# Optimization experiments

Hardware: AMD Instinct MI355X
Metric: run time of the kernel (lower is better)

Reference implementation:

```python
import jax, jax.numpy as jnp
import numpy as np

JOINT = 512
VID_DIM = 1024
K_SIZE = 4
STRIDE = 2
LAYERS = 6
START_LAYER = 1
MARGIN = 0.2
NMS_K = 5          # greedy NMS picks per (query, video) row
NMS_THRESH = 0.7   # IoU suppression threshold
NEG = -1e9


def l2norm(x, axis=-1, eps=1e-8):
    return x / (jnp.linalg.norm(x, axis=axis, keepdims=True) + eps)


def conv1d(x, w, stride):
    # x: [B, C, T], w: [O, I, K] -> [B, O, T']
    return jax.lax.conv_general_dilated(
        x, w, (stride,), 'VALID', dimension_numbers=('NCH', 'OIH', 'NCH'))


def setup_inputs() -> dict:
    key = jax.random.key(0)
    ks = jax.random.split(key, 12)
    B, T, L = 32, 256, 20
    # proposal count P from the valid-conv pyramid
    t, P = T, 0
    for i in range(LAYERS):
        t = (t - K_SIZE) // STRIDE + 1
        if i >= START_LAYER - 1:
            P += t
    video = jax.random.normal(ks[0], (B, T, VID_DIM), jnp.float32)
    words = jax.random.normal(ks[1], (B, L, JOINT), jnp.float32)
    w_masks = jnp.ones((B, L), jnp.bool_)
    lam = jax.random.uniform(ks[2], (1,), jnp.float32)
    iou = jax.random.uniform(ks[3], (P, P), jnp.float32)
    iou_map = 0.5 * (iou + iou.T)  # symmetric pairwise IoU
    scale = 0.02
    fc_w = scale * jax.random.normal(ks[4], (JOINT, VID_DIM), jnp.float32)
    fc_b = jnp.zeros((JOINT,), jnp.float32)
    conv_w = scale * jax.random.normal(ks[5], (LAYERS, JOINT, JOINT, K_SIZE), jnp.float32)
    conv_b = jnp.zeros((LAYERS, JOINT), jnp.float32)
    pw = scale * jax.random.normal(ks[6], (JOINT, JOINT, 1), jnp.float32)
    pb = jnp.zeros((JOINT,), jnp.float32)
    return {'video': video, 'words': words, 'w_masks': w_masks, 'lam': lam,
            'iou_map': iou_map, 'fc_w': fc_w, 'fc_b': fc_b,
            'conv_w': conv_w, 'conv_b': conv_b, 'pw': pw, 'pb': pb}


def diag_loss(scores, margin):
    b = scores.shape[0]
    d = jnp.diag(scores)[:, None]
    cost_s = jnp.clip(margin + scores - d, 0.0)
    cost_im = jnp.clip(margin + scores - d.T, 0.0)
    eye = jnp.eye(b, dtype=bool)
    cost_s = jnp.where(eye, 0.0, cost_s)
    cost_im = jnp.where(eye, 0.0, cost_im)
    return cost_s.sum() / b + cost_im.sum() / b


def _forward(video, words, w_masks, lam, iou_map, fc_w, fc_b, conv_w, conv_b, pw, pb):
    v = jnp.einsum('btv,jv->btj', video, fc_w) + fc_b      # fc: [B,T,J]
    v = jnp.transpose(v, (0, 2, 1))                         # [B,J,T]
    sims = []
    for li in range(LAYERS):
        v = jax.nn.relu(conv1d(v, conv_w[li], STRIDE) + conv_b[li][None, :, None])
        if li >= START_LAYER - 1:
            f = conv1d(v, pw, 1) + pb[None, :, None]        # conv_1d projection
            f = jnp.transpose(f, (0, 2, 1))                 # [B,Tl,J]
            # frame_by_word: frames attend to each query's words (all pairs at once)
            att = jnp.einsum('btd,qld->qbtl', f, words)     # [Q,B,Tl,L]
            att = jnp.where(w_masks[:, None, None, :], att, NEG)
            att = jax.nn.softmax(att, axis=-1)
            v_s = jnp.einsum('qbtl,qld->qbtd', att, words)  # [Q,B,Tl,J]
            sim = jnp.sum(l2norm(f)[None] * l2norm(v_s), axis=-1)  # cosine, [Q,B,Tl]
            sims.append(sim)
    score = jnp.concatenate(sims, axis=-1)                  # [Q,B,P]
    B = score.shape[0]
    positive_map = score[jnp.arange(B), jnp.arange(B)]      # [B,P]
    lam0 = lam[0]

    def nms_row(row):  # greedy temporal NMS scoring over P proposals
        def step(s, k):
            idx = jnp.argmax(s)
            val = jnp.max(s)
            w = lam0 ** k.astype(jnp.float32)
            s = jnp.where(iou_map[idx] > NMS_THRESH, NEG, s)
            s = s.at[idx].set(NEG)
            return s, val * w
        _, vals = jax.lax.scan(step, row, jnp.arange(NMS_K))
        return jnp.sum(vals) / NMS_K

    scores_mat = jax.vmap(jax.vmap(nms_row))(score)         # [Q,B]
    loss = diag_loss(scores_mat, MARGIN)
    return loss, positive_map


def reference(video, words, w_masks, lam, iou_map, fc_w, fc_b, conv_w, conv_b, pw, pb):
    return _forward(video, words, w_masks, lam, iou_map, fc_w, fc_b, conv_w, conv_b, pw, pb)
```

## Files before the change

kernel.cpp:

```cpp
#include <hip/hip_runtime.h>
#include <math.h>

#define B_   32
#define T0_  256
#define J_   512
#define V_   1024
#define Q_   32
#define L_   20
#define P_   241
#define NEG_ (-1e9f)

typedef __attribute__((ext_vector_type(8))) _Float16 half8;
typedef __attribute__((ext_vector_type(4))) _Float16 half4v;
typedef __attribute__((ext_vector_type(4))) float f32x4;

template<int BM, int EPI>
__global__ __launch_bounds__(256) void g1p(
    const _Float16* __restrict__ AH, const _Float16* __restrict__ BH,
    const float* __restrict__ bias,
    _Float16* __restrict__ outH, float* __restrict__ outF,
    int MROWS, int TDIV, int SB, int S0, int TMUL, int BSTR,
    int KLEN, int MP, int OSB, int OS0, int NS) {
  constexpr int FM = BM / 32;
  constexpr int APT = BM / 32;
  constexpr int TPRA = 256 / BM;
  __shared__ _Float16 aS[BM * 72], bS[64 * 72];

  const int tid = threadIdx.x;
  const int m0 = blockIdx.x * BM, n0 = blockIdx.y * 64;
  const int k00 = blockIdx.z * KLEN;
  const int wave = tid >> 6, lane = tid & 63;
  const int wm = (wave >> 1) * (BM / 2), wn = (wave & 1) * 32;
  const int fr = lane & 15, fq = lane >> 4;

  const int arow = tid / TPRA;
  const int acol = (tid % TPRA) * (APT * 8);
  const int brow = tid >> 2, bcol = (tid & 3) * 16;

  const int gm = m0 + arow;
  const bool mval = gm < MROWS;
  const int b2g = gm / TDIV, t2g = gm - b2g * TDIV;
  const size_t aoff = (size_t)(b2g * SB + S0 + t2g * TMUL) * 512;
  const size_t boff = (size_t)(n0 + brow) * (size_t)BSTR;

  f32x4 acc[FM][2];
  #pragma unroll
  for (int i = 0; i < FM; ++i) {
    acc[i][0] = (f32x4)0.f;
    acc[i][1] = (f32x4)0.f;
  }

  half8 z;
  #pragma unroll
  for (int j = 0; j < 8; ++j) z[j] = (_Float16)0.f;

  half8 rA[APT], rB[2];
  auto load = [&](int it) {
    const int k = k00 + it * 64;
    if (mval) {
      #pragma unroll
      for (int i = 0; i < APT; ++i)
        rA[i] = *reinterpret_cast<const half8*>(&AH[aoff + k + acol + i * 8]);
    } else {
      #pragma unroll
      for (int i = 0; i < APT; ++i) rA[i] = z;
    }
    rB[0] = *reinterpret_cast<const half8*>(&BH[boff + k + bcol]);
    rB[1] = *reinterpret_cast<const half8*>(&BH[boff + k + bcol + 8]);
  };

  load(0);
  const int NI = KLEN >> 6;

  for (int it = 0; it < NI; ++it) {
    __syncthreads();
    #pragma unroll
    for (int i = 0; i < APT; ++i)
      *reinterpret_cast<half8*>(&aS[arow * 72 + acol + i * 8]) = rA[i];
    *reinterpret_cast<half8*>(&bS[brow * 72 + bcol]) = rB[0];
    *reinterpret_cast<half8*>(&bS[brow * 72 + bcol + 8]) = rB[1];
    __syncthreads();
    if (it + 1 < NI) load(it + 1);

    #pragma unroll
    for (int ks = 0; ks < 2; ++ks) {
      const int ko = ks * 32 + fq * 8;
      half8 a[FM], b[2];
      #pragma unroll
      for (int mt = 0; mt < FM; ++mt)
        a[mt] = *reinterpret_cast<const half8*>(&aS[(wm + mt * 16 + fr) * 72 + ko]);
      b[0] = *reinterpret_cast<const half8*>(&bS[(wn + fr) * 72 + ko]);
      b[1] = *reinterpret_cast<const half8*>(&bS[(wn + 16 + fr) * 72 + ko]);
      #pragma unroll
      for (int mt = 0; mt < FM; ++mt) {
        acc[mt][0] = __builtin_amdgcn_mfma_f32_16x16x32_f16(a[mt], b[0], acc[mt][0], 0, 0, 0);
        acc[mt][1] = __builtin_amdgcn_mfma_f32_16x16x32_f16(a[mt], b[1], acc[mt][1], 0, 0, 0);
      }
    }
  }

  #pragma unroll
  for (int mt = 0; mt < FM; ++mt) {
    const int mB2 = m0 + wm + mt * 16 + fq * 4;
    #pragma unroll
    for (int nt = 0; nt < 2; ++nt) {
      const int n = n0 + wn + nt * 16 + fr;
      f32x4 c = acc[mt][nt];
      #pragma unroll
      for (int r = 0; r < 4; ++r) {
        const int m = mB2 + r;
        if (m < MROWS) {
          if (EPI == 3) {
            outF[((size_t)blockIdx.z * MP + m) * 512 + n] = c[r];
          } else if (EPI == 2) {
            outF[(size_t)m * NS + n] = c[r];
          } else {
            float x = c[r] + bias[n];
            if (EPI == 1) x = fmaxf(x, 0.f);
            const int bb2 = m / TDIV, tt2 = m - bb2 * TDIV;
            const int orow = bb2 * OSB + OS0 + tt2;
            outH[(size_t)orow * 512 + n] = (_Float16)x;
          }
        }
      }
    }
  }
}

__global__ __launch_bounds__(256) void fc1p(
    const float* __restrict__ A, const _Float16* __restrict__ BH,
    const float* __restrict__ bias, _Float16* __restrict__ outH) {
  __shared__ _Float16 aS[128 * 72], bS[64 * 72];
  const int tid = threadIdx.x;
  const int m0 = blockIdx.x * 128, n0 = blockIdx.y * 64;
  const int wave = tid >> 6, lane = tid & 63;
  const int wm = (wave >> 1) * 64, wn = (wave & 1) * 32;
  const int fr = lane & 15, fq = lane >> 4;
  const int arow = tid >> 1, acol = (tid & 1) * 32;
  const int brow = tid >> 2, bcol = (tid & 3) * 16;
  const size_t aoff = (size_t)(m0 + arow) * 1024;
  const size_t boff = (size_t)(n0 + brow) * 1024;

  f32x4 acc[4][2];
  #pragma unroll
  for (int i = 0; i < 4; ++i) { acc[i][0] = (f32x4)0.f; acc[i][1] = (f32x4)0.f; }

  float4 rAf[8];
  half8 rB[2];
  auto load = [&](int it) {
    const int k = it * 64;
    const float* pa = &A[aoff + k + acol];
    #pragma unroll
    for (int i = 0; i < 8; ++i) rAf[i] = *reinterpret_cast<const float4*>(pa + i * 4);
    rB[0] = *reinterpret_cast<const half8*>(&BH[boff + k + bcol]);
    rB[1] = *reinterpret_cast<const half8*>(&BH[boff + k + bcol + 8]);
  };

  load(0);
  for (int it = 0; it < 16; ++it) {
    __syncthreads();
    #pragma unroll
    for (int g = 0; g < 4; ++g) {
      float tf[8];
      *reinterpret_cast<float4*>(tf) = rAf[2 * g];
      *reinterpret_cast<float4*>(tf + 4) = rAf[2 * g + 1];
      half8 h8;
      #pragma unroll
      for (int j = 0; j < 8; ++j) h8[j] = (_Float16)tf[j];
      *reinterpret_cast<half8*>(&aS[arow * 72 + acol + g * 8]) = h8;
    }
    *reinterpret_cast<half8*>(&bS[brow * 72 + bcol]) = rB[0];
    *reinterpret_cast<half8*>(&bS[brow * 72 + bcol + 8]) = rB[1];
    __syncthreads();
    if (it + 1 < 16) load(it + 1);

    #pragma unroll
    for (int ks = 0; ks < 2; ++ks) {
      const int ko = ks * 32 + fq * 8;
      half8 a[4], b[2];
      #pragma unroll
      for (int mt = 0; mt < 4; ++mt)
        a[mt] = *reinterpret_cast<const half8*>(&aS[(wm + mt * 16 + fr) * 72 + ko]);
      b[0] = *reinterpret_cast<const half8*>(&bS[(wn + fr) * 72 + ko]);
      b[1] = *reinterpret_cast<const half8*>(&bS[(wn + 16 + fr) * 72 + ko]);
      #pragma unroll
      for (int mt = 0; mt < 4; ++mt) {
        acc[mt][0] = __builtin_amdgcn_mfma_f32_16x16x32_f16(a[mt], b[0], acc[mt][0], 0, 0, 0);
        acc[mt][1] = __builtin_amdgcn_mfma_f32_16x16x32_f16(a[mt], b[1], acc[mt][1], 0, 0, 0);
      }
    }
  }

  #pragma unroll
  for (int mt = 0; mt < 4; ++mt) {
    const int mB2 = m0 + wm + mt * 16 + fq * 4;
    #pragma unroll
    for (int nt = 0; nt < 2; ++nt) {
      const int n = n0 + wn + nt * 16 + fr;
      f32x4 c = acc[mt][nt];
      #pragma unroll
      for (int r = 0; r < 4; ++r) {
        const int m = mB2 + r;
        outH[(size_t)m * 512 + n] = (_Float16)(c[r] + bias[n]);
      }
    }
  }
}

__global__ __launch_bounds__(256) void reduce_kernel(
    const float* __restrict__ part, const float* __restrict__ bias,
    _Float16* __restrict__ outH,
    int kS, int MROWS, int MP, int Tl, int Poff) {
  int idx = blockIdx.x * 256 + threadIdx.x;
  if (idx >= MROWS * 512) return;
  int m = idx >> 9, n = idx & 511;
  float s = 0.f;
  for (int ks = 0; ks < kS; ++ks) s += part[((size_t)ks * MP + m) * 512 + n];
  float x = fmaxf(s + bias[n], 0.f);
  int b2 = m / Tl, t2 = m - b2 * Tl;
  int orow = b2 * P_ + Poff + t2;
  outH[(size_t)orow * 512 + n] = (_Float16)x;
}

__global__ __launch_bounds__(256) void split_h(
    const float* __restrict__ a, const float* __restrict__ b,
    const float* __restrict__ c,
    _Float16* __restrict__ oa, _Float16* __restrict__ ob,
    _Float16* __restrict__ oc) {
  int i = blockIdx.x * 256 + threadIdx.x;
  const float* src; _Float16* dst; int off;
  if (i < 131072)      { src = a; dst = oa; off = i; }
  else if (i < 196608) { src = b; dst = ob; off = i - 131072; }
  else if (i < 278528) { src = c; dst = oc; off = i - 196608; }
  else return;
  float4 v = *reinterpret_cast<const float4*>(&src[(size_t)off * 4]);
  half4v h;
  h[0] = (_Float16)v.x; h[1] = (_Float16)v.y;
  h[2] = (_Float16)v.z; h[3] = (_Float16)v.w;
  *reinterpret_cast<half4v*>(&dst[(size_t)off * 4]) = h;
}

__global__ __launch_bounds__(256) void repack_h(
    const float* __restrict__ w, _Float16* __restrict__ oh) {
  int e = blockIdx.x * 256 + threadIdx.x;
  if (e >= 6 * 512 * 512) return;
  float4 v = *reinterpret_cast<const float4*>(&w[(size_t)e * 4]);
  int li = e >> 18, rem = e & 262143, o = rem >> 9, i = rem & 511;
  size_t rb = ((size_t)(li * 512 + o)) * 2048 + i;
  oh[rb]        = (_Float16)v.x;
  oh[rb + 512]  = (_Float16)v.y;
  oh[rb + 1024] = (_Float16)v.z;
  oh[rb + 1536] = (_Float16)v.w;
}

__global__ __launch_bounds__(256) void fnorm_kernel(
    const _Float16* __restrict__ fH, float* __restrict__ fn) {
  int gw = (blockIdx.x * 256 + threadIdx.x) >> 6;
  int lane = threadIdx.x & 63;
  if (gw >= B_ * P_) return;
  half8 h = *reinterpret_cast<const half8*>(&fH[(size_t)gw * 512 + lane * 8]);
  float s = 0.f;
  #pragma unroll
  for (int j = 0; j < 8; ++j) {
    float x = (float)h[j];
    s += x * x;
  }
  #pragma unroll
  for (int off = 32; off; off >>= 1) s += __shfl_xor(s, off);
  if (lane == 0) fn[gw] = sqrtf(s);
}

__global__ __launch_bounds__(256) void gram_kernel(
    const float* __restrict__ words, float* __restrict__ gram) {
  __shared__ float wsh[L_][513];
  int q = blockIdx.x, tid = threadIdx.x;
  for (int idx = tid; idx < L_ * 512; idx += 256)
    wsh[idx >> 9][idx & 511] = words[(size_t)q * L_ * J_ + idx];
  __syncthreads();
  for (int pr = tid; pr < L_ * L_; pr += 256) {
    int l = pr / L_, l2 = pr % L_;
    float sum = 0.f;
    for (int d = 0; d < J_; ++d) sum += wsh[l][d] * wsh[l2][d];
    gram[q * L_ * L_ + pr] = sum;
  }
}

__global__ __launch_bounds__(256) void sim_kernel(
    const float* __restrict__ logits, const float* __restrict__ gram,
    const float* __restrict__ fnorm, float* __restrict__ score) {
  int idx = blockIdx.x * 256 + threadIdx.x;
  if (idx >= Q_ * B_ * P_) return;
  int q = idx / (B_ * P_);
  int r = idx - q * (B_ * P_);
  const float* lg = &logits[(size_t)r * (Q_ * L_) + q * L_];
  float raw[L_], e[L_];
  float m = -1e30f;
  #pragma unroll
  for (int l = 0; l < L_; ++l) { raw[l] = lg[l]; m = fmaxf(m, raw[l]); }
  float s = 0.f;
  #pragma unroll
  for (int l = 0; l < L_; ++l) { e[l] = __expf(raw[l] - m); s += e[l]; }
  float inv = 1.f / s;
  float fvs = 0.f;
  #pragma unroll
  for (int l = 0; l < L_; ++l) fvs += e[l] * raw[l];
  fvs *= inv;
  const float* G = &gram[q * L_ * L_];
  float vn2 = 0.f;
  for (int l = 0; l < L_; ++l) {
    float acc = 0.f;
    #pragma unroll
    for (int l2 = 0; l2 < L_; ++l2) acc += e[l2] * G[l * L_ + l2];
    vn2 += e[l] * acc;
  }
  vn2 *= inv * inv;
  float fn = fnorm[r] + 1e-8f;
  float vn = sqrtf(fmaxf(vn2, 0.f)) + 1e-8f;
  score[idx] = fvs / (fn * vn);
}

__global__ __launch_bounds__(256) void nms_kernel(
    const float* __restrict__ score, const float* __restrict__ iou,
    const float* __restrict__ lam, float* __restrict__ smat) {
  int wid = (blockIdx.x * 256 + threadIdx.x) >> 6;
  int lane = threadIdx.x & 63;
  if (wid >= Q_ * B_) return;
  const float* srow = &score[(size_t)wid * P_];
  float s[4];
  #pragma unroll
  for (int i = 0; i < 4; ++i) {
    int p = lane + 64 * i;
    s[i] = (p < P_) ? srow[p] : NEG_;
  }
  float lamv = lam[0];
  float acc = 0.f, wgt = 1.f;
  for (int k = 0; k < 5; ++k) {
    float bv = NEG_ * 2.f; int bi = 1 << 30;
    #pragma unroll
    for (int i = 0; i < 4; ++i) {
      int p = lane + 64 * i;
      if (s[i] > bv) { bv = s[i]; bi = p; }
    }
    for (int off = 32; off; off >>= 1) {
      float ov = __shfl_xor(bv, off);
      int oi = __shfl_xor(bi, off);
      if (ov > bv || (ov == bv && oi < bi)) { bv = ov; bi = oi; }
    }
    acc += bv * wgt;
    wgt *= lamv;
    const float* irow = &iou[(size_t)bi * P_];
    #pragma unroll
    for (int i = 0; i < 4; ++i) {
      int p = lane + 64 * i;
      if (p < P_ && irow[p] > 0.7f) s[i] = NEG_;
      if (p == bi) s[i] = NEG_;
    }
  }
  if (lane == 0) smat[wid] = acc * 0.2f;
}

__global__ __launch_bounds__(256) void posmap_kernel(
    const float* __restrict__ score, float* __restrict__ out) {
  int idx = blockIdx.x * 256 + threadIdx.x;
  if (idx >= B_ * P_) return;
  int b = idx / P_, p = idx - b * P_;
  out[1 + idx] = score[((size_t)(b * B_ + b)) * P_ + p];
}

__global__ __launch_bounds__(1024) void loss_kernel(
    const float* __restrict__ smat, float* __restrict__ out) {
  __shared__ float sm[B_][B_ + 1];
  __shared__ float red[16];
  int tid = threadIdx.x;
  sm[tid >> 5][tid & 31] = smat[tid];
  __syncthreads();
  int i = tid >> 5, j = tid & 31;
  float val = 0.f;
  if (i != j) {
    float sij = sm[i][j];
    val = fmaxf(0.f, 0.2f + sij - sm[i][i]) + fmaxf(0.f, 0.2f + sij - sm[j][j]);
  }
  #pragma unroll
  for (int off = 32; off; off >>= 1) val += __shfl_xor(val, off);
  if ((tid & 63) == 0) red[tid >> 6] = val;
  __syncthreads();
  if (tid == 0) {
    float t = 0.f;
    #pragma unroll
    for (int w = 0; w < 16; ++w) t += red[w];
    out[0] = t / 32.f;
  }
}

extern "C" void kernel_launch(void* const* d_in, const int* in_sizes, int n_in,
                              void* d_out, int out_size, void* d_ws, size_t ws_size,
                              hipStream_t stream) {
  const float* video  = (const float*)d_in[0];
  const float* words  = (const float*)d_in[1];
  const float* lam    = (const float*)d_in[3];
  const float* iou    = (const float*)d_in[4];
  const float* fc_w   = (const float*)d_in[5];
  const float* fc_b   = (const float*)d_in[6];
  const float* conv_w = (const float*)d_in[7];
  const float* conv_b = (const float*)d_in[8];
  const float* pw     = (const float*)d_in[9];
  const float* pb     = (const float*)d_in[10];
  float* out = (float*)d_out;

  char* base = (char*)d_ws;
  _Float16* fcoH  = (_Float16*)(base + 0);
  _Float16* pyrH  = (_Float16*)(base + 8388608);
  _Float16* fallH = (_Float16*)(base + 16285696);
  _Float16* cwH   = (_Float16*)(base + 24182784);
  _Float16* fcwH  = (_Float16*)(base + 36765696);
  _Float16* pwH   = (_Float16*)(base + 37814272);
  _Float16* wordsH= (_Float16*)(base + 38338560);
  float*    logits= (float*)(base + 38993920);
  float*    part  = (float*)(base + 38993920);
  float*    score = (float*)(base + 58736640);
  float*    fnorm = (float*)(base + 59723776);
  float*    gram  = (float*)(base + 59755520);
  float*    smat  = (float*)(base + 59806720);

  const int Tl[6]   = {127, 62, 30, 14, 6, 2};
  const int Poff[6] = {0, 127, 189, 219, 233, 239};

  split_h<<<1088, 256, 0, stream>>>(fc_w, pw, words, fcwH, pwH, wordsH);
  repack_h<<<6144, 256, 0, stream>>>(conv_w, cwH);

  fc1p<<<dim3(64, 8), 256, 0, stream>>>(video, fcwH, fc_b, fcoH);

  g1p<64, 1><<<dim3(64, 8, 1), 256, 0, stream>>>(
      fcoH, cwH, conv_b, pyrH, nullptr,
      4064, 127, 256, 0, 2, 2048, 2048, 0, P_, 0, 512);

  const int Ms[5]    = {1984, 960, 448, 192, 64};
  const int mbs[5]   = {31, 15, 7, 3, 1};
  const int kSs[5]   = {2, 4, 4, 8, 8};
  const int KLENs[5] = {1024, 512, 512, 256, 256};
  for (int i = 0; i < 5; ++i) {
    int li = i + 1;
    g1p<64, 3><<<dim3(mbs[i], 8, kSs[i]), 256, 0, stream>>>(
        pyrH, cwH + (size_t)li * 512 * 2048, nullptr, nullptr, part,
        Ms[i], Tl[li], P_, Poff[li - 1], 2, 2048, KLENs[i], Ms[i], 0, 0, 512);
    reduce_kernel<<<Ms[i] * 2, 256, 0, stream>>>(
        part, conv_b + li * 512, pyrH, kSs[i], Ms[i], Ms[i], Tl[li], Poff[li]);
  }

  g1p<128, 0><<<dim3(61, 8, 1), 256, 0, stream>>>(
      pyrH, pwH, pb, fallH, nullptr,
      B_ * P_, B_ * P_, 0, 0, 1, 512, 512, 0, 0, 0, 512);

  fnorm_kernel<<<1928, 256, 0, stream>>>(fallH, fnorm);
  gram_kernel<<<Q_, 256, 0, stream>>>(words, gram);
  g1p<128, 2><<<dim3(61, 10, 1), 256, 0, stream>>>(
      fallH, wordsH, nullptr, nullptr, logits,
      B_ * P_, B_ * P_, 0, 0, 1, 512, 512, 0, 0, 0, 640);

  sim_kernel<<<964, 256, 0, stream>>>(logits, gram, fnorm, score);

  nms_kernel<<<256, 256, 0, stream>>>(score, iou, lam, smat);
  posmap_kernel<<<31, 256, 0, stream>>>(score, out);
  loss_kernel<<<1, 1024, 0, stream>>>(smat, out);
}
```

Before: 213.8 us.

## Generalize GEMM K-chunk to 128, replace fused-convert FC GEMM with pre-conversion

The GEMM kernel gains a K-chunk template parameter and an explicit A row stride. All GEMMs now use 128-wide K chunks, which halves the number of barrier/load iterations. The special FC kernel that converted fp32 video on the fly is removed. Instead a separate pass converts video to fp16, and the generic GEMM then runs with BM=64 over a larger grid. The projection and logits GEMMs also switch from BM=128 to BM=64, giving twice as many blocks. In exchange there is an extra 32MB read plus 16MB write for the conversion, and shared memory use per block doubles.

```diff
diff --git a/kernel.cpp b/kernel.cpp
--- a/kernel.cpp
+++ b/kernel.cpp
@@ -14,17 +14,21 @@
 typedef __attribute__((ext_vector_type(4))) _Float16 half4v;
 typedef __attribute__((ext_vector_type(4))) float f32x4;
 
-template<int BM, int EPI>
+template<int BM, int KCH, int EPI>
 __global__ __launch_bounds__(256) void g1p(
     const _Float16* __restrict__ AH, const _Float16* __restrict__ BH,
     const float* __restrict__ bias,
     _Float16* __restrict__ outH, float* __restrict__ outF,
-    int MROWS, int TDIV, int SB, int S0, int TMUL, int BSTR,
+    int MROWS, int TDIV, int SB, int S0, int TMUL, int ASTR, int BSTR,
     int KLEN, int MP, int OSB, int OS0, int NS) {
   constexpr int FM = BM / 32;
-  constexpr int APT = BM / 32;
+  constexpr int LSTR = KCH + 8;
   constexpr int TPRA = 256 / BM;
-  __shared__ _Float16 aS[BM * 72], bS[64 * 72];
+  constexpr int AW = KCH / TPRA;
+  constexpr int AU = AW / 8;
+  constexpr int BW = KCH / 4;
+  constexpr int BU = BW / 8;
+  __shared__ _Float16 aS[BM * LSTR], bS[64 * LSTR];
 
   const int tid = threadIdx.x;
   const int m0 = blockIdx.x * BM, n0 = blockIdx.y * 64;
@@ -34,63 +38,62 @@
   const int fr = lane & 15, fq = lane >> 4;
 
   const int arow = tid / TPRA;
-  const int acol = (tid % TPRA) * (APT * 8);
-  const int brow = tid >> 2, bcol = (tid & 3) * 16;
+  const int acol = (tid % TPRA) * AW;
+  const int brow = tid >> 2, bcol = (tid & 3) * BW;
 
   const int gm = m0 + arow;
   const bool mval = gm < MROWS;
   const int b2g = gm / TDIV, t2g = gm - b2g * TDIV;
-  const size_t aoff = (size_t)(b2g * SB + S0 + t2g * TMUL) * 512;
+  const size_t aoff = (size_t)(b2g * SB + S0 + t2g * TMUL) * (size_t)ASTR;
   const size_t boff = (size_t)(n0 + brow) * (size_t)BSTR;
 
   f32x4 acc[FM][2];
   #pragma unroll
-  for (int i = 0; i < FM; ++i) {
-    acc[i][0] = (f32x4)0.f;
-    acc[i][1] = (f32x4)0.f;
-  }
+  for (int i = 0; i < FM; ++i) { acc[i][0] = (f32x4)0.f; acc[i][1] = (f32x4)0.f; }
 
   half8 z;
   #pragma unroll
   for (int j = 0; j < 8; ++j) z[j] = (_Float16)0.f;
 
-  half8 rA[APT], rB[2];
+  half8 rA[AU], rB[BU];
   auto load = [&](int it) {
-    const int k = k00 + it * 64;
+    const int k = k00 + it * KCH;
     if (mval) {
       #pragma unroll
-      for (int i = 0; i < APT; ++i)
+      for (int i = 0; i < AU; ++i)
         rA[i] = *reinterpret_cast<const half8*>(&AH[aoff + k + acol + i * 8]);
     } else {
       #pragma unroll
-      for (int i = 0; i < APT; ++i) rA[i] = z;
-    }
-    rB[0] = *reinterpret_cast<const half8*>(&BH[boff + k + bcol]);
-    rB[1] = *reinterpret_cast<const half8*>(&BH[boff + k + bcol + 8]);
+      for (int i = 0; i < AU; ++i) rA[i] = z;
+    }
+    #pragma unroll
+    for (int i = 0; i < BU; ++i)
+      rB[i] = *reinterpret_cast<const half8*>(&BH[boff + k + bcol + i * 8]);
   };
 
   load(0);
-  const int NI = KLEN >> 6;
+  const int NI = KLEN / KCH;
 
   for (int it = 0; it < NI; ++it) {
     __syncthreads();
     #pragma unroll
-    for (int i = 0; i < APT; ++i)
-      *reinterpret_cast<half8*>(&aS[arow * 72 + acol + i * 8]) = rA[i];
-    *reinterpret_cast<half8*>(&bS[brow * 72 + bcol]) = rB[0];
-    *reinterpret_cast<half8*>(&bS[brow * 72 + bcol + 8]) = rB[1];
+    for (int i = 0; i < AU; ++i)
+      *reinterpret_cast<half8*>(&aS[arow * LSTR + acol + i * 8]) = rA[i];
+    #pragma unroll
+    for (int i = 0; i < BU; ++i)
+      *reinterpret_cast<half8*>(&bS[brow * LSTR + bcol + i * 8]) = rB[i];
     __syncthreads();
     if (it + 1 < NI) load(it + 1);
 
     #pragma unroll
-    for (int ks = 0; ks < 2; ++ks) {
+    for (int ks = 0; ks < KCH / 32; ++ks) {
       const int ko = ks * 32 + fq * 8;
       half8 a[FM], b[2];
       #pragma unroll
       for (int mt = 0; mt < FM; ++mt)
-        a[mt] = *reinterpret_cast<const half8*>(&aS[(wm + mt * 16 + fr) * 72 + ko]);
-      b[0] = *reinterpret_cast<const half8*>(&bS[(wn + fr) * 72 + ko]);
-      b[1] = *reinterpret_cast<const half8*>(&bS[(wn + 16 + fr) * 72 + ko]);
+        a[mt] = *reinterpret_cast<const half8*>(&aS[(wm + mt * 16 + fr) * LSTR + ko]);
+      b[0] = *reinterpret_cast<const half8*>(&bS[(wn + fr) * LSTR + ko]);
+      b[1] = *reinterpret_cast<const half8*>(&bS[(wn + 16 + fr) * LSTR + ko]);
       #pragma unroll
       for (int mt = 0; mt < FM; ++mt) {
         acc[mt][0] = __builtin_amdgcn_mfma_f32_16x16x32_f16(a[mt], b[0], acc[mt][0], 0, 0, 0);
@@ -127,83 +130,14 @@
   }
 }
 
-__global__ __launch_bounds__(256) void fc1p(
-    const float* __restrict__ A, const _Float16* __restrict__ BH,
-    const float* __restrict__ bias, _Float16* __restrict__ outH) {
-  __shared__ _Float16 aS[128 * 72], bS[64 * 72];
-  const int tid = threadIdx.x;
-  const int m0 = blockIdx.x * 128, n0 = blockIdx.y * 64;
-  const int wave = tid >> 6, lane = tid & 63;
-  const int wm = (wave >> 1) * 64, wn = (wave & 1) * 32;
-  const int fr = lane & 15, fq = lane >> 4;
-  const int arow = tid >> 1, acol = (tid & 1) * 32;
-  const int brow = tid >> 2, bcol = (tid & 3) * 16;
-  const size_t aoff = (size_t)(m0 + arow) * 1024;
-  const size_t boff = (size_t)(n0 + brow) * 1024;
-
-  f32x4 acc[4][2];
-  #pragma unroll
-  for (int i = 0; i < 4; ++i) { acc[i][0] = (f32x4)0.f; acc[i][1] = (f32x4)0.f; }
-
-  float4 rAf[8];
-  half8 rB[2];
-  auto load = [&](int it) {
-    const int k = it * 64;
-    const float* pa = &A[aoff + k + acol];
-    #pragma unroll
-    for (int i = 0; i < 8; ++i) rAf[i] = *reinterpret_cast<const float4*>(pa + i * 4);
-    rB[0] = *reinterpret_cast<const half8*>(&BH[boff + k + bcol]);
-    rB[1] = *reinterpret_cast<const half8*>(&BH[boff + k + bcol + 8]);
-  };
-
-  load(0);
-  for (int it = 0; it < 16; ++it) {
-    __syncthreads();
-    #pragma unroll
-    for (int g = 0; g < 4; ++g) {
-      float tf[8];
-      *reinterpret_cast<float4*>(tf) = rAf[2 * g];
-      *reinterpret_cast<float4*>(tf + 4) = rAf[2 * g + 1];
-      half8 h8;
-      #pragma unroll
-      for (int j = 0; j < 8; ++j) h8[j] = (_Float16)tf[j];
-      *reinterpret_cast<half8*>(&aS[arow * 72 + acol + g * 8]) = h8;
-    }
-    *reinterpret_cast<half8*>(&bS[brow * 72 + bcol]) = rB[0];
-    *reinterpret_cast<half8*>(&bS[brow * 72 + bcol + 8]) = rB[1];
-    __syncthreads();
-    if (it + 1 < 16) load(it + 1);
-
-    #pragma unroll
-    for (int ks = 0; ks < 2; ++ks) {
-      const int ko = ks * 32 + fq * 8;
-      half8 a[4], b[2];
-      #pragma unroll
-      for (int mt = 0; mt < 4; ++mt)
-        a[mt] = *reinterpret_cast<const half8*>(&aS[(wm + mt * 16 + fr) * 72 + ko]);
-      b[0] = *reinterpret_cast<const half8*>(&bS[(wn + fr) * 72 + ko]);
-      b[1] = *reinterpret_cast<const half8*>(&bS[(wn + 16 + fr) * 72 + ko]);
-      #pragma unroll
-      for (int mt = 0; mt < 4; ++mt) {
-        acc[mt][0] = __builtin_amdgcn_mfma_f32_16x16x32_f16(a[mt], b[0], acc[mt][0], 0, 0, 0);
-        acc[mt][1] = __builtin_amdgcn_mfma_f32_16x16x32_f16(a[mt], b[1], acc[mt][1], 0, 0, 0);
-      }
-    }
-  }
-
-  #pragma unroll
-  for (int mt = 0; mt < 4; ++mt) {
-    const int mB2 = m0 + wm + mt * 16 + fq * 4;
-    #pragma unroll
-    for (int nt = 0; nt < 2; ++nt) {
-      const int n = n0 + wn + nt * 16 + fr;
-      f32x4 c = acc[mt][nt];
-      #pragma unroll
-      for (int r = 0; r < 4; ++r) {
-        const int m = mB2 + r;
-        outH[(size_t)m * 512 + n] = (_Float16)(c[r] + bias[n]);
-      }
-    }
+__global__ __launch_bounds__(256) void cvt_video(
+    const float* __restrict__ in, _Float16* __restrict__ oh) {
+  for (int i = blockIdx.x * 256 + threadIdx.x; i < 2097152; i += 2048 * 256) {
+    float4 v = *reinterpret_cast<const float4*>(&in[(size_t)i * 4]);
+    half4v h;
+    h[0] = (_Float16)v.x; h[1] = (_Float16)v.y;
+    h[2] = (_Float16)v.z; h[3] = (_Float16)v.w;
+    *reinterpret_cast<half4v*>(&oh[(size_t)i * 4]) = h;
   }
 }
 
@@ -408,31 +342,35 @@
   float* out = (float*)d_out;
 
   char* base = (char*)d_ws;
-  _Float16* fcoH  = (_Float16*)(base + 0);
-  _Float16* pyrH  = (_Float16*)(base + 8388608);
-  _Float16* fallH = (_Float16*)(base + 16285696);
-  _Float16* cwH   = (_Float16*)(base + 24182784);
-  _Float16* fcwH  = (_Float16*)(base + 36765696);
-  _Float16* pwH   = (_Float16*)(base + 37814272);
-  _Float16* wordsH= (_Float16*)(base + 38338560);
-  float*    logits= (float*)(base + 38993920);
-  float*    part  = (float*)(base + 38993920);
-  float*    score = (float*)(base + 58736640);
-  float*    fnorm = (float*)(base + 59723776);
-  float*    gram  = (float*)(base + 59755520);
-  float*    smat  = (float*)(base + 59806720);
+  _Float16* videoH= (_Float16*)(base + 0);
+  _Float16* fcoH  = (_Float16*)(base + 16777216);
+  _Float16* pyrH  = (_Float16*)(base + 25165824);
+  _Float16* fallH = (_Float16*)(base + 33062912);
+  _Float16* cwH   = (_Float16*)(base + 40960000);
+  _Float16* fcwH  = (_Float16*)(base + 53542912);
+  _Float16* pwH   = (_Float16*)(base + 54591488);
+  _Float16* wordsH= (_Float16*)(base + 55115776);
+  float*    logits= (float*)(base + 55771136);
+  float*    part  = (float*)(base + 55771136);
+  float*    score = (float*)(base + 75513856);
+  float*    fnorm = (float*)(base + 76500992);
+  float*    gram  = (float*)(base + 76532736);
+  float*    smat  = (float*)(base + 76583936);
 
   const int Tl[6]   = {127, 62, 30, 14, 6, 2};
   const int Poff[6] = {0, 127, 189, 219, 233, 239};
 
+  cvt_video<<<2048, 256, 0, stream>>>(video, videoH);
   split_h<<<1088, 256, 0, stream>>>(fc_w, pw, words, fcwH, pwH, wordsH);
   repack_h<<<6144, 256, 0, stream>>>(conv_w, cwH);
 
-  fc1p<<<dim3(64, 8), 256, 0, stream>>>(video, fcwH, fc_b, fcoH);
-
-  g1p<64, 1><<<dim3(64, 8, 1), 256, 0, stream>>>(
+  g1p<64, 128, 0><<<dim3(128, 8), 256, 0, stream>>>(
+      videoH, fcwH, fc_b, fcoH, nullptr,
+      8192, 8192, 0, 0, 1, 1024, 1024, 1024, 0, 0, 0, 512);
+
+  g1p<64, 128, 1><<<dim3(64, 8, 1), 256, 0, stream>>>(
       fcoH, cwH, conv_b, pyrH, nullptr,
-      4064, 127, 256, 0, 2, 2048, 2048, 0, P_, 0, 512);
+      4064, 127, 256, 0, 2, 512, 2048, 2048, 0, P_, 0, 512);
 
   const int Ms[5]    = {1984, 960, 448, 192, 64};
   const int mbs[5]   = {31, 15, 7, 3, 1};
@@ -440,22 +378,22 @@
   const int KLENs[5] = {1024, 512, 512, 256, 256};
   for (int i = 0; i < 5; ++i) {
     int li = i + 1;
-    g1p<64, 3><<<dim3(mbs[i], 8, kSs[i]), 256, 0, stream>>>(
+    g1p<64, 128, 3><<<dim3(mbs[i], 8, kSs[i]), 256, 0, stream>>>(
         pyrH, cwH + (size_t)li * 512 * 2048, nullptr, nullptr, part,
-        Ms[i], Tl[li], P_, Poff[li - 1], 2, 2048, KLENs[i], Ms[i], 0, 0, 512);
+        Ms[i], Tl[li], P_, Poff[li - 1], 2, 512, 2048, KLENs[i], Ms[i], 0, 0, 512);
     reduce_kernel<<<Ms[i] * 2, 256, 0, stream>>>(
         part, conv_b + li * 512, pyrH, kSs[i], Ms[i], Ms[i], Tl[li], Poff[li]);
   }
 
-  g1p<128, 0><<<dim3(61, 8, 1), 256, 0, stream>>>(
+  g1p<64, 128, 0><<<dim3(121, 8, 1), 256, 0, stream>>>(
       pyrH, pwH, pb, fallH, nullptr,
-      B_ * P_, B_ * P_, 0, 0, 1, 512, 512, 0, 0, 0, 512);
+      B_ * P_, B_ * P_, 0, 0, 1, 512, 512, 512, 0, 0, 0, 512);
 
   fnorm_kernel<<<1928, 256, 0, stream>>>(fallH, fnorm);
   gram_kernel<<<Q_, 256, 0, stream>>>(words, gram);
-  g1p<128, 2><<<dim3(61, 10, 1), 256, 0, stream>>>(
+  g1p<64, 128, 2><<<dim3(121, 10, 1), 256, 0, stream>>>(
       fallH, wordsH, nullptr, nullptr, logits,
-      B_ * P_, B_ * P_, 0, 0, 1, 512, 512, 0, 0, 0, 640);
+      B_ * P_, B_ * P_, 0, 0, 1, 512, 512, 512, 0, 0, 0, 640);
 
   sim_kernel<<<964, 256, 0, stream>>>(logits, gram, fnorm, score);
 
```

Result: faster. 206.0 us (-3.7%).
